# Kernel tuning notes

Hardware: AMD Instinct MI355X
Metric: run time of the kernel (lower is better)

Reference implementation:

```python
import jax, jax.numpy as jnp
import numpy as np

EPSILON = 0.001
CAP = 2000.0
H, W, C, B = 224, 224, 1024, 256


def setup_inputs() -> dict:
    key = jax.random.key(0)
    k1, k2, k3, k4 = jax.random.split(key, 4)
    x = jax.random.normal(k1, (B, H, W), dtype=jnp.float32)
    positions = 0.5 + 0.3 * jax.random.normal(k2, (1, 1, C, 2), dtype=jnp.float32)
    sigmas = 0.02 * jax.random.normal(k3, (1, 1, C), dtype=jnp.float32)
    curve_weights = 0.2 * jax.random.normal(k4, (1, 1, C), dtype=jnp.float32)
    y_axis = jnp.linspace(0.0, 1.0, H + 1)[:-1]
    x_axis = jnp.linspace(0.0, 1.0, W + 1)[:-1]
    ys, xs = jnp.meshgrid(y_axis, x_axis, indexing='ij')
    return {"x": x, "positions": positions, "sigmas": sigmas,
            "curve_weights": curve_weights, "xs": xs.astype(jnp.float32),
            "ys": ys.astype(jnp.float32)}


def calc_curves(positions, sigmas, curve_weights, xs, ys):
    # sigmas/curve_weights: (1,1,C); xs/ys: (H,W)
    two_sig2 = 2.0 * sigmas ** 2 + EPSILON            # (1,1,C)
    factor = 1.0 / (2.0 * jnp.pi * sigmas ** 2 + EPSILON)
    grid = (xs[:, :, None] - positions[..., 1]) ** 2 + \
           (ys[:, :, None] - positions[..., 0]) ** 2   # (H,W,C)
    curves = factor * jnp.exp(-grid / two_sig2) * curve_weights
    return jnp.clip(curves, -CAP, CAP)                 # (H,W,C)


def reference(x, positions, sigmas, curve_weights, xs, ys):
    x = x.reshape(-1, H, W)
    curves = calc_curves(positions, sigmas, curve_weights, xs, ys)
    num_pixels = float(H * W)
    # sum over H,W of curves[None] * x[...,None]  ==  GEMM contraction
    out = jnp.einsum('bhw,hwc->bc', x, curves) / num_pixels
    return out
```

## Files before the change

kernel.cpp:

```cpp
#include <hip/hip_runtime.h>
#include <hip/hip_bf16.h>
#include <stdint.h>

#define HH 224
#define WW 224
#define CC 1024
#define BB 256
#define KK (HH*WW)
#define EPSILON_F 0.001f
#define LOG2E 1.4426950408889634f
#define INVN (1.0f/50176.0f)
#define CLAMP_V (2000.0f/50176.0f)

#define KCHUNKS 32
#define ROWS_PER_CHUNK 7
#define STEPS 49

#define LDS_STRIDE 36

typedef __bf16 bf16x8 __attribute__((ext_vector_type(8)));
typedef float  f32x4  __attribute__((ext_vector_type(4)));

__global__ __launch_bounds__(256)
void cvt_bf16_kernel(const float* __restrict__ x, __hip_bfloat16* __restrict__ xb, int n8) {
    int i = blockIdx.x * 256 + threadIdx.x;
    if (i >= n8) return;
    const float4* p = (const float4*)(x + (size_t)i * 8);
    float4 a = p[0], b = p[1];
    union { __hip_bfloat16 h[8]; uint4 u; } o;
    o.h[0] = (__hip_bfloat16)a.x; o.h[1] = (__hip_bfloat16)a.y;
    o.h[2] = (__hip_bfloat16)a.z; o.h[3] = (__hip_bfloat16)a.w;
    o.h[4] = (__hip_bfloat16)b.x; o.h[5] = (__hip_bfloat16)b.y;
    o.h[6] = (__hip_bfloat16)b.z; o.h[7] = (__hip_bfloat16)b.w;
    *(uint4*)(xb + (size_t)i * 8) = o.u;
}

__global__ __launch_bounds__(256)
void reduce_kernel(const float* __restrict__ part, float* __restrict__ out) {
    int i = blockIdx.x * 256 + threadIdx.x;
    const f32x4* p = (const f32x4*)part + i;
    f32x4 s = {0.f, 0.f, 0.f, 0.f};
#pragma unroll
    for (int z = 0; z < KCHUNKS; ++z)
        s += p[(size_t)z * (BB * CC / 4)];
    ((f32x4*)out)[i] = s;
}

template <bool BF16A, bool PARTIAL>
__global__ __launch_bounds__(256)
void blob_gemm_kernel(const void* __restrict__ xin,
                      const float* __restrict__ pos,
                      const float* __restrict__ sig,
                      const float* __restrict__ cwt,
                      const float* __restrict__ xs,
                      const float* __restrict__ ys,
                      float* __restrict__ dst) {
    __shared__ __bf16 Bs[2][64 * LDS_STRIDE];
    __shared__ float  xrow[WW];
    __shared__ float  ycol[ROWS_PER_CHUNK];

    const int tid  = threadIdx.x;
    const int wave = tid >> 6;
    const int lane = tid & 63;

    const int n  = blockIdx.x;
    const int j  = n >> 3;
    const int z  = (n & 7) * 4 + (j >> 4);
    const int c0 = (j & 15) * 64;
    const int k0 = z * (ROWS_PER_CHUNK * WW);

    if (tid < WW) xrow[tid] = xs[tid];
    if (tid >= WW && tid < WW + ROWS_PER_CHUNK)
        ycol[tid - WW] = ys[(z * ROWS_PER_CHUNK + (tid - WW)) * WW];

    const int q   = tid & 3;
    const int cr0 = tid >> 2;
    const int c   = c0 + cr0;
    float A2, S2, P0, P1;
    {
        float s  = sig[c];
        float w  = cwt[c];
        float s2 = s * s;
        A2 = w / (6.283185307179586f * s2 + EPSILON_F) * INVN;
        S2 = LOG2E / (2.0f * s2 + EPSILON_F);
        P0 = pos[2 * c];
        P1 = pos[2 * c + 1];
    }
    const bool doClamp = __any(fabsf(A2) > CLAMP_V) != 0;

    const int bs_w = cr0 * LDS_STRIDE + q * 8;

    const int wm = wave * 64;
    const int fl = lane & 15;
    const int fk = (lane >> 4) * 8;
    const int br_off = fl * LDS_STRIDE + fk;

    const __hip_bfloat16* afb[4];
    const float* aff[4];
#pragma unroll
    for (int mi = 0; mi < 4; ++mi) {
        size_t off = (size_t)(wm + fl + mi * 16) * KK + k0 + fk;
        afb[mi] = (const __hip_bfloat16*)xin + off;
        aff[mi] = (const float*)xin + off;
    }

    f32x4 acc[4][4];
#pragma unroll
    for (int i = 0; i < 4; ++i)
#pragma unroll
        for (int jj = 0; jj < 4; ++jj) acc[i][jj] = (f32x4){0.f, 0.f, 0.f, 0.f};

    __syncthreads();

    float ycolr[ROWS_PER_CHUNK];
#pragma unroll
    for (int r = 0; r < ROWS_PER_CHUNK; ++r) ycolr[r] = ycol[r];

    bf16x8 fa[4];
#pragma unroll
    for (int mi = 0; mi < 4; ++mi) {
        if (BF16A) {
            fa[mi] = *(const bf16x8*)(afb[mi]);
        } else {
            float4 f0 = *(const float4*)(aff[mi]);
            float4 f1 = *(const float4*)(aff[mi] + 4);
            bf16x8 t;
            t[0] = (__bf16)f0.x; t[1] = (__bf16)f0.y; t[2] = (__bf16)f0.z; t[3] = (__bf16)f0.w;
            t[4] = (__bf16)f1.x; t[5] = (__bf16)f1.y; t[6] = (__bf16)f1.z; t[7] = (__bf16)f1.w;
            fa[mi] = t;
        }
    }
    float Ex[8];
    {
        float4 xv0 = *(const float4*)(xrow + q * 8);
        float4 xv1 = *(const float4*)(xrow + q * 8 + 4);
        float xv[8] = {xv0.x, xv0.y, xv0.z, xv0.w, xv1.x, xv1.y, xv1.z, xv1.w};
#pragma unroll
        for (int i = 0; i < 8; ++i) {
            float dx = xv[i] - P1;
            Ex[i] = __builtin_amdgcn_exp2f(-(dx * S2 * dx));
        }
        float dy  = ycolr[0] - P0;
        float eyA = __builtin_amdgcn_exp2f(-(dy * S2 * dy)) * A2;
        float v[8];
#pragma unroll
        for (int i = 0; i < 8; ++i) v[i] = Ex[i] * eyA;
        if (doClamp) {
#pragma unroll
            for (int i = 0; i < 8; ++i) v[i] = fminf(fmaxf(v[i], -CLAMP_V), CLAMP_V);
        }
        union { __bf16 h[8]; uint4 u; } cv;
#pragma unroll
        for (int i = 0; i < 8; ++i) cv.h[i] = (__bf16)v[i];
        *(uint4*)(&Bs[0][bs_w]) = cv.u;
    }
    __syncthreads();

    int nr = 1, nwb = 0;
#pragma unroll 2
    for (int s = 0; s < STEPS; ++s) {
        const int cb = s & 1;

        uint4  pa[4];
        float4 pf0[4], pf1[4];
        if (s < STEPS - 1) {
            const int koff = nr * WW + nwb * 32;
            if (BF16A) {
#pragma unroll
                for (int mi = 0; mi < 4; ++mi) pa[mi] = *(const uint4*)(afb[mi] + koff);
            } else {
#pragma unroll
                for (int mi = 0; mi < 4; ++mi) {
                    pf0[mi] = *(const float4*)(aff[mi] + koff);
                    pf1[mi] = *(const float4*)(aff[mi] + koff + 4);
                }
            }
        }

        bf16x8 fb[4];
#pragma unroll
        for (int i = 0; i < 4; ++i)
            fb[i] = *(const bf16x8*)(&Bs[cb][br_off + i * 16 * LDS_STRIDE]);

        if (s < STEPS - 1) {
            if (nr == 0) {
                float4 xv0 = *(const float4*)(xrow + nwb * 32 + q * 8);
                float4 xv1 = *(const float4*)(xrow + nwb * 32 + q * 8 + 4);
                float xv[8] = {xv0.x, xv0.y, xv0.z, xv0.w, xv1.x, xv1.y, xv1.z, xv1.w};
#pragma unroll
                for (int i = 0; i < 8; ++i) {
                    float dx = xv[i] - P1;
                    Ex[i] = __builtin_amdgcn_exp2f(-(dx * S2 * dx));
                }
            }
            float dy  = ycolr[nr] - P0;
            float eyA = __builtin_amdgcn_exp2f(-(dy * S2 * dy)) * A2;
            float v[8];
#pragma unroll
            for (int i = 0; i < 8; ++i) v[i] = Ex[i] * eyA;
            if (doClamp) {
#pragma unroll
                for (int i = 0; i < 8; ++i) v[i] = fminf(fmaxf(v[i], -CLAMP_V), CLAMP_V);
            }
            union { __bf16 h[8]; uint4 u; } cv;
#pragma unroll
            for (int i = 0; i < 8; ++i) cv.h[i] = (__bf16)v[i];
            *(uint4*)(&Bs[cb ^ 1][bs_w]) = cv.u;
            ++nr;
            if (nr == ROWS_PER_CHUNK) { nr = 0; ++nwb; }
        }

#pragma unroll
        for (int mi = 0; mi < 4; ++mi)
#pragma unroll
            for (int ni = 0; ni < 4; ++ni)
                acc[mi][ni] = __builtin_amdgcn_mfma_f32_16x16x32_bf16(
                    fa[mi], fb[ni], acc[mi][ni], 0, 0, 0);

        if (s < STEPS - 1) {
            if (BF16A) {
#pragma unroll
                for (int mi = 0; mi < 4; ++mi) {
                    union { uint4 u; bf16x8 h; } t; t.u = pa[mi];
                    fa[mi] = t.h;
                }
            } else {
#pragma unroll
                for (int mi = 0; mi < 4; ++mi) {
                    bf16x8 t;
                    t[0] = (__bf16)pf0[mi].x; t[1] = (__bf16)pf0[mi].y;
                    t[2] = (__bf16)pf0[mi].z; t[3] = (__bf16)pf0[mi].w;
                    t[4] = (__bf16)pf1[mi].x; t[5] = (__bf16)pf1[mi].y;
                    t[6] = (__bf16)pf1[mi].z; t[7] = (__bf16)pf1[mi].w;
                    fa[mi] = t;
                }
            }
        }
        __syncthreads();
    }

    const int orow = (lane >> 4) * 4;
    float* base = PARTIAL ? (dst + (size_t)z * BB * CC) : dst;
#pragma unroll
    for (int mi = 0; mi < 4; ++mi) {
        int m = wm + mi * 16 + orow;
#pragma unroll
        for (int ni = 0; ni < 4; ++ni) {
            int cc = c0 + ni * 16 + fl;
#pragma unroll
            for (int v = 0; v < 4; ++v) {
                if (PARTIAL)
                    base[(size_t)(m + v) * CC + cc] = acc[mi][ni][v];
                else
                    atomicAdd(base + (size_t)(m + v) * CC + cc, acc[mi][ni][v]);
            }
        }
    }
}

extern "C" void kernel_launch(void* const* d_in, const int* in_sizes, int n_in,
                              void* d_out, int out_size, void* d_ws, size_t ws_size,
                              hipStream_t stream) {
    const float* x   = (const float*)d_in[0];
    const float* pos = (const float*)d_in[1];
    const float* sg  = (const float*)d_in[2];
    const float* cw  = (const float*)d_in[3];
    const float* xs  = (const float*)d_in[4];
    const float* ys  = (const float*)d_in[5];
    float* out = (float*)d_out;

    dim3 grid(16 * KCHUNKS);
    const size_t nx   = (size_t)BB * KK;
    const size_t XB   = nx * sizeof(__hip_bfloat16);
    const size_t PART = (size_t)KCHUNKS * BB * CC * 4;
    const int n8 = (int)(nx / 8);

    if (ws_size >= XB + PART) {
        __hip_bfloat16* xb = (__hip_bfloat16*)d_ws;
        float* part = (float*)((char*)d_ws + XB);
        cvt_bf16_kernel<<<(n8 + 255) / 256, 256, 0, stream>>>(x, xb, n8);
        blob_gemm_kernel<true, true><<<grid, 256, 0, stream>>>(xb, pos, sg, cw, xs, ys, part);
        reduce_kernel<<<BB * CC / 4 / 256, 256, 0, stream>>>(part, out);
    } else if (ws_size >= PART) {
        float* part = (float*)d_ws;
        blob_gemm_kernel<false, true><<<grid, 256, 0, stream>>>(x, pos, sg, cw, xs, ys, part);
        reduce_kernel<<<BB * CC / 4 / 256, 256, 0, stream>>>(part, out);
    } else if (ws_size >= XB) {
        __hip_bfloat16* xb = (__hip_bfloat16*)d_ws;
        hipMemsetAsync(out, 0, (size_t)BB * CC * sizeof(float), stream);
        cvt_bf16_kernel<<<(n8 + 255) / 256, 256, 0, stream>>>(x, xb, n8);
        blob_gemm_kernel<true, false><<<grid, 256, 0, stream>>>(xb, pos, sg, cw, xs, ys, out);
    } else {
        hipMemsetAsync(out, 0, (size_t)BB * CC * sizeof(float), stream);
        blob_gemm_kernel<false, false><<<grid, 256, 0, stream>>>(x, pos, sg, cw, xs, ys, out);
    }
}
```

Measured before the change: 149.6 us.

## Process two K-steps per barrier with deeper A-prefetch pipeline

```diff
diff --git a/kernel.cpp b/kernel.cpp
--- a/kernel.cpp
+++ b/kernel.cpp
@@ -17,6 +17,8 @@
 #define STEPS 49
 
 #define LDS_STRIDE 36
+#define TILE_E (64 * LDS_STRIDE)
+#define PAIR_E (2 * TILE_E)
 
 typedef __bf16 bf16x8 __attribute__((ext_vector_type(8)));
 typedef float  f32x4  __attribute__((ext_vector_type(4)));
@@ -55,7 +57,7 @@
                       const float* __restrict__ xs,
                       const float* __restrict__ ys,
                       float* __restrict__ dst) {
-    __shared__ __bf16 Bs[2][64 * LDS_STRIDE];
+    __shared__ __bf16 Bs[4 * TILE_E];
     __shared__ float  xrow[WW];
     __shared__ float  ycol[ROWS_PER_CHUNK];
 
@@ -116,31 +118,19 @@
 #pragma unroll
     for (int r = 0; r < ROWS_PER_CHUNK; ++r) ycolr[r] = ycol[r];
 
-    bf16x8 fa[4];
-#pragma unroll
-    for (int mi = 0; mi < 4; ++mi) {
-        if (BF16A) {
-            fa[mi] = *(const bf16x8*)(afb[mi]);
-        } else {
-            float4 f0 = *(const float4*)(aff[mi]);
-            float4 f1 = *(const float4*)(aff[mi] + 4);
-            bf16x8 t;
-            t[0] = (__bf16)f0.x; t[1] = (__bf16)f0.y; t[2] = (__bf16)f0.z; t[3] = (__bf16)f0.w;
-            t[4] = (__bf16)f1.x; t[5] = (__bf16)f1.y; t[6] = (__bf16)f1.z; t[7] = (__bf16)f1.w;
-            fa[mi] = t;
-        }
-    }
     float Ex[8];
-    {
-        float4 xv0 = *(const float4*)(xrow + q * 8);
-        float4 xv1 = *(const float4*)(xrow + q * 8 + 4);
-        float xv[8] = {xv0.x, xv0.y, xv0.z, xv0.w, xv1.x, xv1.y, xv1.z, xv1.w};
-#pragma unroll
-        for (int i = 0; i < 8; ++i) {
-            float dx = xv[i] - P1;
-            Ex[i] = __builtin_amdgcn_exp2f(-(dx * S2 * dx));
-        }
-        float dy  = ycolr[0] - P0;
+    auto stageB = [&](int row, int wb, int wrElem) {
+        if (row == 0) {
+            float4 xv0 = *(const float4*)(xrow + wb * 32 + q * 8);
+            float4 xv1 = *(const float4*)(xrow + wb * 32 + q * 8 + 4);
+            float xv[8] = {xv0.x, xv0.y, xv0.z, xv0.w, xv1.x, xv1.y, xv1.z, xv1.w};
+#pragma unroll
+            for (int i = 0; i < 8; ++i) {
+                float dx = xv[i] - P1;
+                Ex[i] = __builtin_amdgcn_exp2f(-(dx * S2 * dx));
+            }
+        }
+        float dy  = ycolr[row] - P0;
         float eyA = __builtin_amdgcn_exp2f(-(dy * S2 * dy)) * A2;
         float v[8];
 #pragma unroll
@@ -152,91 +142,157 @@
         union { __bf16 h[8]; uint4 u; } cv;
 #pragma unroll
         for (int i = 0; i < 8; ++i) cv.h[i] = (__bf16)v[i];
-        *(uint4*)(&Bs[0][bs_w]) = cv.u;
-    }
+        *(uint4*)(&Bs[wrElem + bs_w]) = cv.u;
+    };
+
+    auto loadA = [&](int koff, bf16x8* dstFrag) {
+#pragma unroll
+        for (int mi = 0; mi < 4; ++mi) {
+            if (BF16A) {
+                dstFrag[mi] = *(const bf16x8*)(afb[mi] + koff);
+            } else {
+                float4 f0 = *(const float4*)(aff[mi] + koff);
+                float4 f1 = *(const float4*)(aff[mi] + koff + 4);
+                bf16x8 t;
+                t[0] = (__bf16)f0.x; t[1] = (__bf16)f0.y; t[2] = (__bf16)f0.z; t[3] = (__bf16)f0.w;
+                t[4] = (__bf16)f1.x; t[5] = (__bf16)f1.y; t[6] = (__bf16)f1.z; t[7] = (__bf16)f1.w;
+                dstFrag[mi] = t;
+            }
+        }
+    };
+
+    uint4  pa0[4], pa1[4];
+    float4 pf00[4], pf01[4], pf10[4], pf11[4];
+
+    auto issue0 = [&](int koff) {
+        if (BF16A) {
+#pragma unroll
+            for (int mi = 0; mi < 4; ++mi) pa0[mi] = *(const uint4*)(afb[mi] + koff);
+        } else {
+#pragma unroll
+            for (int mi = 0; mi < 4; ++mi) {
+                pf00[mi] = *(const float4*)(aff[mi] + koff);
+                pf01[mi] = *(const float4*)(aff[mi] + koff + 4);
+            }
+        }
+    };
+    auto issue1 = [&](int koff) {
+        if (BF16A) {
+#pragma unroll
+            for (int mi = 0; mi < 4; ++mi) pa1[mi] = *(const uint4*)(afb[mi] + koff);
+        } else {
+#pragma unroll
+            for (int mi = 0; mi < 4; ++mi) {
+                pf10[mi] = *(const float4*)(aff[mi] + koff);
+                pf11[mi] = *(const float4*)(aff[mi] + koff + 4);
+            }
+        }
+    };
+    auto commit0 = [&](bf16x8* dstFrag) {
+        if (BF16A) {
+#pragma unroll
+            for (int mi = 0; mi < 4; ++mi) {
+                union { uint4 u; bf16x8 h; } t; t.u = pa0[mi];
+                dstFrag[mi] = t.h;
+            }
+        } else {
+#pragma unroll
+            for (int mi = 0; mi < 4; ++mi) {
+                bf16x8 t;
+                t[0] = (__bf16)pf00[mi].x; t[1] = (__bf16)pf00[mi].y;
+                t[2] = (__bf16)pf00[mi].z; t[3] = (__bf16)pf00[mi].w;
+                t[4] = (__bf16)pf01[mi].x; t[5] = (__bf16)pf01[mi].y;
+                t[6] = (__bf16)pf01[mi].z; t[7] = (__bf16)pf01[mi].w;
+                dstFrag[mi] = t;
+            }
+        }
+    };
+    auto commit1 = [&](bf16x8* dstFrag) {
+        if (BF16A) {
+#pragma unroll
+            for (int mi = 0; mi < 4; ++mi) {
+                union { uint4 u; bf16x8 h; } t; t.u = pa1[mi];
+                dstFrag[mi] = t.h;
+            }
+        } else {
+#pragma unroll
+            for (int mi = 0; mi < 4; ++mi) {
+                bf16x8 t;
+                t[0] = (__bf16)pf10[mi].x; t[1] = (__bf16)pf10[mi].y;
+                t[2] = (__bf16)pf10[mi].z; t[3] = (__bf16)pf10[mi].w;
+                t[4] = (__bf16)pf11[mi].x; t[5] = (__bf16)pf11[mi].y;
+                t[6] = (__bf16)pf11[mi].z; t[7] = (__bf16)pf11[mi].w;
+                dstFrag[mi] = t;
+            }
+        }
+    };
+
+    bf16x8 fa0[4], fa1[4];
+    loadA(0, fa0);
+    loadA(WW, fa1);
+    issue0(2 * WW);
+    issue1(3 * WW);
+    stageB(0, 0, 0);
+    stageB(1, 0, TILE_E);
     __syncthreads();
 
-    int nr = 1, nwb = 0;
-#pragma unroll 2
-    for (int s = 0; s < STEPS; ++s) {
-        const int cb = s & 1;
-
-        uint4  pa[4];
-        float4 pf0[4], pf1[4];
-        if (s < STEPS - 1) {
-            const int koff = nr * WW + nwb * 32;
-            if (BF16A) {
-#pragma unroll
-                for (int mi = 0; mi < 4; ++mi) pa[mi] = *(const uint4*)(afb[mi] + koff);
-            } else {
-#pragma unroll
-                for (int mi = 0; mi < 4; ++mi) {
-                    pf0[mi] = *(const float4*)(aff[mi] + koff);
-                    pf1[mi] = *(const float4*)(aff[mi] + koff + 4);
-                }
-            }
-        }
-
-        bf16x8 fb[4];
-#pragma unroll
-        for (int i = 0; i < 4; ++i)
-            fb[i] = *(const bf16x8*)(&Bs[cb][br_off + i * 16 * LDS_STRIDE]);
-
-        if (s < STEPS - 1) {
-            if (nr == 0) {
-                float4 xv0 = *(const float4*)(xrow + nwb * 32 + q * 8);
-                float4 xv1 = *(const float4*)(xrow + nwb * 32 + q * 8 + 4);
-                float xv[8] = {xv0.x, xv0.y, xv0.z, xv0.w, xv1.x, xv1.y, xv1.z, xv1.w};
-#pragma unroll
-                for (int i = 0; i < 8; ++i) {
-                    float dx = xv[i] - P1;
-                    Ex[i] = __builtin_amdgcn_exp2f(-(dx * S2 * dx));
-                }
-            }
-            float dy  = ycolr[nr] - P0;
-            float eyA = __builtin_amdgcn_exp2f(-(dy * S2 * dy)) * A2;
-            float v[8];
-#pragma unroll
-            for (int i = 0; i < 8; ++i) v[i] = Ex[i] * eyA;
-            if (doClamp) {
-#pragma unroll
-                for (int i = 0; i < 8; ++i) v[i] = fminf(fmaxf(v[i], -CLAMP_V), CLAMP_V);
-            }
-            union { __bf16 h[8]; uint4 u; } cv;
-#pragma unroll
-            for (int i = 0; i < 8; ++i) cv.h[i] = (__bf16)v[i];
-            *(uint4*)(&Bs[cb ^ 1][bs_w]) = cv.u;
-            ++nr;
-            if (nr == ROWS_PER_CHUNK) { nr = 0; ++nwb; }
-        }
+    int nr = 2, nwb = 0;
+    int rdE = 0;
+#pragma unroll 1
+    for (int r = 0; r < 24; ++r) {
+        bf16x8 fb0[4], fb1[4];
+#pragma unroll
+        for (int i = 0; i < 4; ++i) {
+            fb0[i] = *(const bf16x8*)(&Bs[rdE + br_off + i * 16 * LDS_STRIDE]);
+            fb1[i] = *(const bf16x8*)(&Bs[rdE + TILE_E + br_off + i * 16 * LDS_STRIDE]);
+        }
+
+        const int t0r = nr, t0b = nwb;
+        int t1r = t0r + 1, t1b = t0b;
+        if (t1r == ROWS_PER_CHUNK) { t1r = 0; ++t1b; }
+        nr = t1r + 1; nwb = t1b;
+        if (nr == ROWS_PER_CHUNK) { nr = 0; ++nwb; }
+        int u1r = nr + 1, u1b = nwb;
+        if (u1r == ROWS_PER_CHUNK) { u1r = 0; ++u1b; }
+
+        const int wrE = rdE ^ PAIR_E;
+        stageB(t0r, t0b, wrE);
+        if (r < 23) stageB(t1r, t1b, wrE + TILE_E);
 
 #pragma unroll
         for (int mi = 0; mi < 4; ++mi)
 #pragma unroll
             for (int ni = 0; ni < 4; ++ni)
                 acc[mi][ni] = __builtin_amdgcn_mfma_f32_16x16x32_bf16(
-                    fa[mi], fb[ni], acc[mi][ni], 0, 0, 0);
-
-        if (s < STEPS - 1) {
-            if (BF16A) {
-#pragma unroll
-                for (int mi = 0; mi < 4; ++mi) {
-                    union { uint4 u; bf16x8 h; } t; t.u = pa[mi];
-                    fa[mi] = t.h;
-                }
-            } else {
-#pragma unroll
-                for (int mi = 0; mi < 4; ++mi) {
-                    bf16x8 t;
-                    t[0] = (__bf16)pf0[mi].x; t[1] = (__bf16)pf0[mi].y;
-                    t[2] = (__bf16)pf0[mi].z; t[3] = (__bf16)pf0[mi].w;
-                    t[4] = (__bf16)pf1[mi].x; t[5] = (__bf16)pf1[mi].y;
-                    t[6] = (__bf16)pf1[mi].z; t[7] = (__bf16)pf1[mi].w;
-                    fa[mi] = t;
-                }
-            }
-        }
+                    fa0[mi], fb0[ni], acc[mi][ni], 0, 0, 0);
+#pragma unroll
+        for (int mi = 0; mi < 4; ++mi)
+#pragma unroll
+            for (int ni = 0; ni < 4; ++ni)
+                acc[mi][ni] = __builtin_amdgcn_mfma_f32_16x16x32_bf16(
+                    fa1[mi], fb1[ni], acc[mi][ni], 0, 0, 0);
+
+        commit0(fa0);
+        commit1(fa1);
+
+        if (r <= 22) issue0(nr * WW + nwb * 32);
+        if (r <= 21) issue1(u1r * WW + u1b * 32);
+
         __syncthreads();
+        rdE ^= PAIR_E;
+    }
+
+    {
+        bf16x8 fbL[4];
+#pragma unroll
+        for (int i = 0; i < 4; ++i)
+            fbL[i] = *(const bf16x8*)(&Bs[rdE + br_off + i * 16 * LDS_STRIDE]);
+#pragma unroll
+        for (int mi = 0; mi < 4; ++mi)
+#pragma unroll
+            for (int ni = 0; ni < 4; ++ni)
+                acc[mi][ni] = __builtin_amdgcn_mfma_f32_16x16x32_bf16(
+                    fa0[mi], fbL[ni], acc[mi][ni], 0, 0, 0);
     }
 
     const int orow = (lane >> 4) * 4;
```

Measured after the change: 173.6 us. 1.16x slower.

## Fuse bf16 conversion, GEMM and split-K reduction into one persistent kernel

Applied to the files above, without the earlier changes.

```diff
diff --git a/kernel.cpp b/kernel.cpp
--- a/kernel.cpp
+++ b/kernel.cpp
@@ -17,6 +17,9 @@
 #define STEPS 49
 
 #define LDS_STRIDE 36
+
+#define NBLK 512
+#define OCT_PER_BLK 3136
 
 typedef __bf16 bf16x8 __attribute__((ext_vector_type(8)));
 typedef float  f32x4  __attribute__((ext_vector_type(4)));
@@ -46,6 +49,221 @@
     ((f32x4*)out)[i] = s;
 }
 
+__device__ __forceinline__ void grid_sync(unsigned* cnt, unsigned target) {
+    __syncthreads();
+    if (threadIdx.x == 0) {
+        __hip_atomic_fetch_add(cnt, 1u, __ATOMIC_RELEASE, __HIP_MEMORY_SCOPE_AGENT);
+        while (__hip_atomic_load(cnt, __ATOMIC_ACQUIRE, __HIP_MEMORY_SCOPE_AGENT) < target) {
+            __builtin_amdgcn_s_sleep(2);
+        }
+    }
+    __syncthreads();
+}
+
+__global__ __launch_bounds__(256)
+void fused_blob_kernel(const float* __restrict__ x,
+                       const float* __restrict__ pos,
+                       const float* __restrict__ sig,
+                       const float* __restrict__ cwt,
+                       const float* __restrict__ xs,
+                       const float* __restrict__ ys,
+                       float* __restrict__ out,
+                       __hip_bfloat16* __restrict__ xb,
+                       float* __restrict__ part,
+                       unsigned* __restrict__ cnt) {
+    __shared__ __bf16 Bs[2][64 * LDS_STRIDE];
+    __shared__ float  xrow[WW];
+    __shared__ float  ycol[ROWS_PER_CHUNK];
+
+    const int tid  = threadIdx.x;
+    const int wave = tid >> 6;
+    const int lane = tid & 63;
+
+    {
+        const int base = blockIdx.x * OCT_PER_BLK;
+#pragma unroll 1
+        for (int i = tid; i < OCT_PER_BLK; i += 256) {
+            const int o = base + i;
+            const float4* p = (const float4*)(x + (size_t)o * 8);
+            float4 a = p[0], b = p[1];
+            union { __hip_bfloat16 h[8]; uint4 u; } ov;
+            ov.h[0] = (__hip_bfloat16)a.x; ov.h[1] = (__hip_bfloat16)a.y;
+            ov.h[2] = (__hip_bfloat16)a.z; ov.h[3] = (__hip_bfloat16)a.w;
+            ov.h[4] = (__hip_bfloat16)b.x; ov.h[5] = (__hip_bfloat16)b.y;
+            ov.h[6] = (__hip_bfloat16)b.z; ov.h[7] = (__hip_bfloat16)b.w;
+            *(uint4*)(xb + (size_t)o * 8) = ov.u;
+        }
+    }
+    grid_sync(cnt, NBLK);
+
+    const int n  = blockIdx.x;
+    const int j  = n >> 3;
+    const int z  = (n & 7) * 4 + (j >> 4);
+    const int c0 = (j & 15) * 64;
+    const int k0 = z * (ROWS_PER_CHUNK * WW);
+
+    if (tid < WW) xrow[tid] = xs[tid];
+    if (tid >= WW && tid < WW + ROWS_PER_CHUNK)
+        ycol[tid - WW] = ys[(z * ROWS_PER_CHUNK + (tid - WW)) * WW];
+
+    const int q   = tid & 3;
+    const int cr0 = tid >> 2;
+    const int c   = c0 + cr0;
+    float A2, S2, P0, P1;
+    {
+        float s  = sig[c];
+        float w  = cwt[c];
+        float s2 = s * s;
+        A2 = w / (6.283185307179586f * s2 + EPSILON_F) * INVN;
+        S2 = LOG2E / (2.0f * s2 + EPSILON_F);
+        P0 = pos[2 * c];
+        P1 = pos[2 * c + 1];
+    }
+    const bool doClamp = __any(fabsf(A2) > CLAMP_V) != 0;
+
+    const int bs_w = cr0 * LDS_STRIDE + q * 8;
+
+    const int wm = wave * 64;
+    const int fl = lane & 15;
+    const int fk = (lane >> 4) * 8;
+    const int br_off = fl * LDS_STRIDE + fk;
+
+    const __hip_bfloat16* afb[4];
+#pragma unroll
+    for (int mi = 0; mi < 4; ++mi)
+        afb[mi] = xb + (size_t)(wm + fl + mi * 16) * KK + k0 + fk;
+
+    f32x4 acc[4][4];
+#pragma unroll
+    for (int i = 0; i < 4; ++i)
+#pragma unroll
+        for (int jj = 0; jj < 4; ++jj) acc[i][jj] = (f32x4){0.f, 0.f, 0.f, 0.f};
+
+    __syncthreads();
+
+    float ycolr[ROWS_PER_CHUNK];
+#pragma unroll
+    for (int r = 0; r < ROWS_PER_CHUNK; ++r) ycolr[r] = ycol[r];
+
+    bf16x8 fa[4];
+#pragma unroll
+    for (int mi = 0; mi < 4; ++mi)
+        fa[mi] = *(const bf16x8*)(afb[mi]);
+    float Ex[8];
+    {
+        float4 xv0 = *(const float4*)(xrow + q * 8);
+        float4 xv1 = *(const float4*)(xrow + q * 8 + 4);
+        float xv[8] = {xv0.x, xv0.y, xv0.z, xv0.w, xv1.x, xv1.y, xv1.z, xv1.w};
+#pragma unroll
+        for (int i = 0; i < 8; ++i) {
+            float dx = xv[i] - P1;
+            Ex[i] = __builtin_amdgcn_exp2f(-(dx * S2 * dx));
+        }
+        float dy  = ycolr[0] - P0;
+        float eyA = __builtin_amdgcn_exp2f(-(dy * S2 * dy)) * A2;
+        float v[8];
+#pragma unroll
+        for (int i = 0; i < 8; ++i) v[i] = Ex[i] * eyA;
+        if (doClamp) {
+#pragma unroll
+            for (int i = 0; i < 8; ++i) v[i] = fminf(fmaxf(v[i], -CLAMP_V), CLAMP_V);
+        }
+        union { __bf16 h[8]; uint4 u; } cv;
+#pragma unroll
+        for (int i = 0; i < 8; ++i) cv.h[i] = (__bf16)v[i];
+        *(uint4*)(&Bs[0][bs_w]) = cv.u;
+    }
+    __syncthreads();
+
+    int nr = 1, nwb = 0;
+#pragma unroll 2
+    for (int s = 0; s < STEPS; ++s) {
+        const int cb = s & 1;
+
+        uint4 pa[4];
+        if (s < STEPS - 1) {
+            const int koff = nr * WW + nwb * 32;
+#pragma unroll
+            for (int mi = 0; mi < 4; ++mi) pa[mi] = *(const uint4*)(afb[mi] + koff);
+        }
+
+        bf16x8 fb[4];
+#pragma unroll
+        for (int i = 0; i < 4; ++i)
+            fb[i] = *(const bf16x8*)(&Bs[cb][br_off + i * 16 * LDS_STRIDE]);
+
+        if (s < STEPS - 1) {
+            if (nr == 0) {
+                float4 xv0 = *(const float4*)(xrow + nwb * 32 + q * 8);
+                float4 xv1 = *(const float4*)(xrow + nwb * 32 + q * 8 + 4);
+                float xv[8] = {xv0.x, xv0.y, xv0.z, xv0.w, xv1.x, xv1.y, xv1.z, xv1.w};
+#pragma unroll
+                for (int i = 0; i < 8; ++i) {
+                    float dx = xv[i] - P1;
+                    Ex[i] = __builtin_amdgcn_exp2f(-(dx * S2 * dx));
+                }
+            }
+            float dy  = ycolr[nr] - P0;
+            float eyA = __builtin_amdgcn_exp2f(-(dy * S2 * dy)) * A2;
+            float v[8];
+#pragma unroll
+            for (int i = 0; i < 8; ++i) v[i] = Ex[i] * eyA;
+            if (doClamp) {
+#pragma unroll
+                for (int i = 0; i < 8; ++i) v[i] = fminf(fmaxf(v[i], -CLAMP_V), CLAMP_V);
+            }
+            union { __bf16 h[8]; uint4 u; } cv;
+#pragma unroll
+            for (int i = 0; i < 8; ++i) cv.h[i] = (__bf16)v[i];
+            *(uint4*)(&Bs[cb ^ 1][bs_w]) = cv.u;
+            ++nr;
+            if (nr == ROWS_PER_CHUNK) { nr = 0; ++nwb; }
+        }
+
+#pragma unroll
+        for (int mi = 0; mi < 4; ++mi)
+#pragma unroll
+            for (int ni = 0; ni < 4; ++ni)
+                acc[mi][ni] = __builtin_amdgcn_mfma_f32_16x16x32_bf16(
+                    fa[mi], fb[ni], acc[mi][ni], 0, 0, 0);
+
+        if (s < STEPS - 1) {
+#pragma unroll
+            for (int mi = 0; mi < 4; ++mi) {
+                union { uint4 u; bf16x8 h; } t; t.u = pa[mi];
+                fa[mi] = t.h;
+            }
+        }
+        __syncthreads();
+    }
+
+    const int orow = (lane >> 4) * 4;
+    float* base = part + (size_t)z * BB * CC;
+#pragma unroll
+    for (int mi = 0; mi < 4; ++mi) {
+        int m = wm + mi * 16 + orow;
+#pragma unroll
+        for (int ni = 0; ni < 4; ++ni) {
+            int cc = c0 + ni * 16 + fl;
+#pragma unroll
+            for (int v = 0; v < 4; ++v)
+                base[(size_t)(m + v) * CC + cc] = acc[mi][ni][v];
+        }
+    }
+
+    grid_sync(cnt, 2 * NBLK);
+
+    if (tid < 128) {
+        const int slot = blockIdx.x * 128 + tid;
+        const f32x4* p = (const f32x4*)part + slot;
+        f32x4 s = {0.f, 0.f, 0.f, 0.f};
+#pragma unroll
+        for (int zz = 0; zz < KCHUNKS; ++zz)
+            s += p[(size_t)zz * (BB * CC / 4)];
+        ((f32x4*)out)[slot] = s;
+    }
+}
+
 template <bool BF16A, bool PARTIAL>
 __global__ __launch_bounds__(256)
 void blob_gemm_kernel(const void* __restrict__ xin,
@@ -89,7 +307,6 @@
     const bool doClamp = __any(fabsf(A2) > CLAMP_V) != 0;
 
     const int bs_w = cr0 * LDS_STRIDE + q * 8;
-
     const int wm = wave * 64;
     const int fl = lane & 15;
     const int fk = (lane >> 4) * 8;
@@ -160,7 +377,6 @@
 #pragma unroll 2
     for (int s = 0; s < STEPS; ++s) {
         const int cb = s & 1;
-
         uint4  pa[4];
         float4 pf0[4], pf1[4];
         if (s < STEPS - 1) {
@@ -176,12 +392,10 @@
                 }
             }
         }
-
         bf16x8 fb[4];
 #pragma unroll
         for (int i = 0; i < 4; ++i)
             fb[i] = *(const bf16x8*)(&Bs[cb][br_off + i * 16 * LDS_STRIDE]);
-
         if (s < STEPS - 1) {
             if (nr == 0) {
                 float4 xv0 = *(const float4*)(xrow + nwb * 32 + q * 8);
@@ -209,14 +423,12 @@
             ++nr;
             if (nr == ROWS_PER_CHUNK) { nr = 0; ++nwb; }
         }
-
 #pragma unroll
         for (int mi = 0; mi < 4; ++mi)
 #pragma unroll
             for (int ni = 0; ni < 4; ++ni)
                 acc[mi][ni] = __builtin_amdgcn_mfma_f32_16x16x32_bf16(
                     fa[mi], fb[ni], acc[mi][ni], 0, 0, 0);
-
         if (s < STEPS - 1) {
             if (BF16A) {
 #pragma unroll
@@ -269,13 +481,19 @@
     const float* ys  = (const float*)d_in[5];
     float* out = (float*)d_out;
 
-    dim3 grid(16 * KCHUNKS);
+    dim3 grid(NBLK);
     const size_t nx   = (size_t)BB * KK;
     const size_t XB   = nx * sizeof(__hip_bfloat16);
     const size_t PART = (size_t)KCHUNKS * BB * CC * 4;
     const int n8 = (int)(nx / 8);
 
-    if (ws_size >= XB + PART) {
+    if (ws_size >= XB + PART + 128) {
+        __hip_bfloat16* xb = (__hip_bfloat16*)d_ws;
+        float* part = (float*)((char*)d_ws + XB);
+        unsigned* cnt = (unsigned*)((char*)d_ws + XB + PART);
+        hipMemsetAsync(cnt, 0, 128, stream);
+        fused_blob_kernel<<<grid, 256, 0, stream>>>(x, pos, sg, cw, xs, ys, out, xb, part, cnt);
+    } else if (ws_size >= XB + PART) {
         __hip_bfloat16* xb = (__hip_bfloat16*)d_ws;
         float* part = (float*)((char*)d_ws + XB);
         cvt_bf16_kernel<<<(n8 + 255) / 256, 256, 0, stream>>>(x, xb, n8);
```

Measured after the change: 318.0 us. 113% more time.
